# Kernel tuning notes

Hardware: AMD Instinct MI355X
Metric: run time of the kernel (lower is better)

The kernel has to match this reference:

```python
import jax, jax.numpy as jnp
import numpy as np

B, NA, NB = 4, 2048, 2048
IN_A, IN_B, OUT, H = 128, 128, 128, 8
DH = OUT // H  # 16
NEG = jnp.float32(-1e30)
SLOPE = jnp.float32(0.01)


def setup_inputs() -> dict:
    key = jax.random.key(0)
    ks = jax.random.split(key, 13)
    s = 0.05
    return {
        "h_A": jax.random.normal(ks[0], (B, NA, IN_A), jnp.float32),
        "h_B": jax.random.normal(ks[1], (B, NB, IN_B), jnp.float32),
        "mask": jax.random.randint(ks[2], (B, NA, NB), 0, 2) > 0,
        # per-head params stacked on a leading head axis
        "WA_w": jax.random.normal(ks[3], (H, IN_A, DH), jnp.float32) * s,
        "WA_b": jax.random.normal(ks[4], (H, DH), jnp.float32) * s,
        "WB_w": jax.random.normal(ks[5], (H, IN_B, DH), jnp.float32) * s,
        "WB_b": jax.random.normal(ks[6], (H, DH), jnp.float32) * s,
        "aA_w": jax.random.normal(ks[7], (H, DH), jnp.float32) * s,
        "aA_b": jax.random.normal(ks[8], (H,), jnp.float32) * s,
        "aB_w": jax.random.normal(ks[9], (H, DH), jnp.float32) * s,
        "aB_b": jax.random.normal(ks[10], (H,), jnp.float32) * s,
        "W_w": jax.random.normal(ks[11], (OUT, OUT), jnp.float32) * s,
        "W_b": jax.random.normal(ks[12], (OUT,), jnp.float32) * s,
    }


def _leaky(x):
    return jnp.where(x >= 0, x, SLOPE * x)


def reference(h_A, h_B, mask, WA_w, WA_b, WB_w, WB_b, aA_w, aA_b, aB_w, aB_b, W_w, W_b):
    # per-head linear projections: [B, H, N, DH]
    z_A = jnp.einsum('bni,hid->bhnd', h_A, WA_w) + WA_b[None, :, None, :]
    z_B = jnp.einsum('bmi,hid->bhmd', h_B, WB_w) + WB_b[None, :, None, :]
    # additive attention logits: [B, H, NA] + [B, H, NB] -> [B, H, NA, NB]
    eA = jnp.einsum('bhnd,hd->bhn', z_A, aA_w) + aA_b[None, :, None]
    eB = jnp.einsum('bhmd,hd->bhm', z_B, aB_w) + aB_b[None, :, None]
    e = eA[:, :, :, None] + eB[:, :, None, :]
    m = mask[:, None, :, :]  # broadcast over heads
    e = jnp.where(m, e, NEG)
    alpha = jax.nn.softmax(_leaky(e), axis=-1)
    alpha = jnp.where(m, alpha, jnp.zeros((), alpha.dtype))
    # weighted aggregation: [B, H, NA, DH]
    out_h = jnp.einsum('bhnm,bhmd->bhnd', alpha, z_B)
    # concat heads -> [B, NA, OUT], final projection
    cat = out_h.transpose(0, 2, 1, 3).reshape(h_A.shape[0], h_A.shape[1], H * DH)
    return cat @ W_w.T + W_b
```

## Files before the change

### kernel.cpp

```cpp
#include <hip/hip_runtime.h>

typedef unsigned short u16;
typedef unsigned int u32;
typedef unsigned char u8;

typedef _Float16 f16x8 __attribute__((ext_vector_type(8)));
typedef _Float16 f16x2 __attribute__((ext_vector_type(2)));
typedef __attribute__((ext_vector_type(4))) float f32x4;


#if __has_builtin(__builtin_amdgcn_sbfe)
#define SEXTBIT(m, j) ((u32)__builtin_amdgcn_sbfe((int)(m), (u32)(j), 1u))
#else
#define SEXTBIT(m, j) ((u32)(((int)((m) << (31 - (j)))) >> 31))
#endif

__global__ __launch_bounds__(256) void kzero(float* __restrict__ out){
  out[blockIdx.x * 256 + threadIdx.x] = 0.f;
}

__global__ __launch_bounds__(256) void kmask_f32(const u32* __restrict__ mw,
                                                 u32* __restrict__ Mb){
  int t = threadIdx.x;
  int lane = t & 63;
  int wid = blockIdx.x * 4 + (t >> 6);
  size_t base = (size_t)wid * 2048;
  for (int i = 0; i < 32; i += 4){
    u32 v0 = mw[base + (size_t)(i + 0) * 64 + lane];
    u32 v1 = mw[base + (size_t)(i + 1) * 64 + lane];
    u32 v2 = mw[base + (size_t)(i + 2) * 64 + lane];
    u32 v3 = mw[base + (size_t)(i + 3) * 64 + lane];
    unsigned long long b0 = __ballot(v0 != 0u);
    unsigned long long b1 = __ballot(v1 != 0u);
    unsigned long long b2 = __ballot(v2 != 0u);
    unsigned long long b3 = __ballot(v3 != 0u);
    if (lane == 0){
      size_t o = base / 32 + (size_t)i * 2;
      *(unsigned long long*)&Mb[o + 0] = b0;
      *(unsigned long long*)&Mb[o + 2] = b1;
      *(unsigned long long*)&Mb[o + 4] = b2;
      *(unsigned long long*)&Mb[o + 6] = b3;
    }
  }
}

__global__ __launch_bounds__(256) void kmask_b8(const void* __restrict__ maskv,
                                                u32* __restrict__ Mb){
  int oid = blockIdx.x * 256 + threadIdx.x;
  u32 bits = 0;
  const uint4* mp = (const uint4*)maskv + (size_t)oid * 2;
  uint4 va = mp[0], vb = mp[1];
  u32 w[8] = {va.x, va.y, va.z, va.w, vb.x, vb.y, vb.z, vb.w};
  #pragma unroll
  for (int q = 0; q < 8; ++q)
    #pragma unroll
    for (int bb = 0; bb < 4; ++bb)
      bits |= ((w[q] >> (8 * bb)) & 255u ? 1u : 0u) << (q * 4 + bb);
  Mb[oid] = bits;
}

__global__ __launch_bounds__(256) void kmask_b16(const void* __restrict__ maskv,
                                                 u32* __restrict__ Mb){
  int oid = blockIdx.x * 256 + threadIdx.x;
  u32 bits = 0;
  const uint4* mp = (const uint4*)maskv + (size_t)oid * 4;
  #pragma unroll
  for (int k = 0; k < 4; ++k){
    uint4 v = mp[k];
    u32 w[4] = {v.x, v.y, v.z, v.w};
    #pragma unroll
    for (int q = 0; q < 4; ++q){
      bits |= ((w[q] & 0xFFFFu) ? 1u : 0u) << (k * 8 + q * 2);
      bits |= ((w[q] >> 16)     ? 1u : 0u) << (k * 8 + q * 2 + 1);
    }
  }
  Mb[oid] = bits;
}

__global__ __launch_bounds__(256) void kmask_det(const void* __restrict__ maskv,
                                                 u32* __restrict__ Mb){
  __shared__ int s_aw, s_ab, s_ah;
  int t = threadIdx.x;
  if (t == 0){ s_aw = 1; s_ab = 1; s_ah = 1; }
  __syncthreads();
  {
    const u32* mw = (const u32*)maskv;
    int aw = 1, ah = 1, ab = 1;
    #pragma unroll
    for (int j = 0; j < 4; ++j){
      u32 m = mw[t + 256 * j];
      if (!(m == 0u || m == 1u || m == 0x3F800000u)) aw = 0;
      u32 lo = m & 0xFFFFu, hi = m >> 16;
      if (!((lo == 0u || lo == 1u || lo == 0x3F80u) && (hi == 0u || hi == 1u || hi == 0x3F80u))) ah = 0;
      if (m & ~0x01010101u) ab = 0;
    }
    unsigned long long fa = __ballot(!aw);
    unsigned long long fh = __ballot(!ah);
    unsigned long long fb = __ballot(!ab);
    if ((t & 63) == 0){
      if (fa) atomicAnd(&s_aw, 0);
      if (fh) atomicAnd(&s_ah, 0);
      if (fb) atomicAnd(&s_ab, 0);
    }
  }
  __syncthreads();
  int Fm = 0;
  if (s_aw) Fm = 0; else if (s_ab) Fm = 1; else if (s_ah) Fm = 2;

  if (Fm == 0){
    int lane = t & 63;
    int wid = blockIdx.x * 4 + (t >> 6);
    const u32* mw = (const u32*)maskv;
    size_t base = (size_t)wid * 2048;
    for (int i = 0; i < 32; i += 4){
      u32 v0 = mw[base + (size_t)(i + 0) * 64 + lane];
      u32 v1 = mw[base + (size_t)(i + 1) * 64 + lane];
      u32 v2 = mw[base + (size_t)(i + 2) * 64 + lane];
      u32 v3 = mw[base + (size_t)(i + 3) * 64 + lane];
      unsigned long long b0 = __ballot(v0 != 0u);
      unsigned long long b1 = __ballot(v1 != 0u);
      unsigned long long b2 = __ballot(v2 != 0u);
      unsigned long long b3 = __ballot(v3 != 0u);
      if (lane == 0){
        size_t o = base / 32 + (size_t)i * 2;
        *(unsigned long long*)&Mb[o + 0] = b0;
        *(unsigned long long*)&Mb[o + 2] = b1;
        *(unsigned long long*)&Mb[o + 4] = b2;
        *(unsigned long long*)&Mb[o + 6] = b3;
      }
    }
    return;
  }
  int oid = blockIdx.x * 256 + t;
  u32 bits = 0;
  if (Fm == 1){
    const uint4* mp = (const uint4*)maskv + (size_t)oid * 2;
    #pragma unroll
    for (int k = 0; k < 2; ++k){
      uint4 v = mp[k];
      u32 w[4] = {v.x, v.y, v.z, v.w};
      #pragma unroll
      for (int q = 0; q < 4; ++q)
        #pragma unroll
        for (int bb = 0; bb < 4; ++bb)
          bits |= ((w[q] >> (8*bb)) & 255u ? 1u : 0u) << (k*16 + q*4 + bb);
    }
  } else {
    const uint4* mp = (const uint4*)maskv + (size_t)oid * 4;
    #pragma unroll
    for (int k = 0; k < 4; ++k){
      uint4 v = mp[k];
      u32 w[4] = {v.x, v.y, v.z, v.w};
      #pragma unroll
      for (int q = 0; q < 4; ++q){
        bits |= ((w[q] & 0xFFFFu) ? 1u : 0u) << (k*8 + q*2);
        bits |= ((w[q] >> 16)     ? 1u : 0u) << (k*8 + q*2 + 1);
      }
    }
  }
  Mb[oid] = bits;
}

__global__ __launch_bounds__(256) void kprep(
    const float* __restrict__ hA, const float* __restrict__ hB,
    const float* __restrict__ WAw, const float* __restrict__ WAb,
    const float* __restrict__ aAw, const float* __restrict__ aAb,
    const float* __restrict__ WBw, const float* __restrict__ WBb,
    const float* __restrict__ aBw, const float* __restrict__ aBb,
    const float* __restrict__ Ww, float* __restrict__ WtO,
    uint4* __restrict__ zF,
    float* __restrict__ RA,
    u32* __restrict__ EBh, u32* __restrict__ GBh){
  __shared__ float smem[12416];
  int gid = blockIdx.x, t = threadIdx.x;

  if (gid < 256){
    float* h_l = smem;
    float* W_l = smem + 4224;
    float* T   = smem + 4224;
    int R0 = gid * 32;

    for (int j = 0; j < 4; ++j){
      int idx4 = t + 256 * j;
      int r = idx4 >> 5, k0 = (idx4 & 31) * 4;
      *(float4*)&h_l[r * 132 + k0] = *(const float4*)&hB[(size_t)(R0 + r) * 128 + k0];
    }

    int cg = t & 15, rg = t >> 4;
    float acc[2][8];
    for (int i = 0; i < 2; ++i) for (int s = 0; s < 8; ++s) acc[i][s] = 0.f;

    for (int kc = 0; kc < 2; ++kc){
      __syncthreads();
      for (int j = 0; j < 8; ++j){
        int idx4 = t + 256 * j;
        int k = idx4 >> 5, c0 = (idx4 & 31) * 4;
        *(float4*)&W_l[k * 128 + c0] =
          *(const float4*)&WBw[(size_t)(c0 >> 4) * 2048 + (kc * 64 + k) * 16 + (c0 & 15)];
      }
      __syncthreads();
      for (int k = 0; k < 64; ++k){
        int kk = kc * 64 + k;
        float4 w0 = *(const float4*)&W_l[k * 128 + cg * 8];
        float4 w1 = *(const float4*)&W_l[k * 128 + cg * 8 + 4];
        float wv[8] = {w0.x, w0.y, w0.z, w0.w, w1.x, w1.y, w1.z, w1.w};
        #pragma unroll
        for (int i = 0; i < 2; ++i){
          float hv = h_l[(rg * 2 + i) * 132 + kk];
          #pragma unroll
          for (int s = 0; s < 8; ++s) acc[i][s] = fmaf(hv, wv[s], acc[i][s]);
        }
      }
    }
    __syncthreads();
    for (int i = 0; i < 2; ++i)
      #pragma unroll
      for (int s = 0; s < 8; ++s)
        T[(cg * 8 + s) * 33 + rg * 2 + i] = acc[i][s] + WBb[cg * 8 + s];
    __syncthreads();

    int b = R0 >> 11;
    int mblk = (R0 & 2047) >> 5;
    for (int it = t; it < 512; it += 256){
      int h = it >> 6, lane = it & 63;
      int d = lane & 15, mq = (lane >> 4) * 8;
      const float* Tp = &T[(h * 16 + d) * 33 + mq];
      u32 wv2[4];
      #pragma unroll
      for (int p = 0; p < 4; ++p){
        union { f16x2 h2; u32 u; } c;
        c.h2 = (f16x2){(_Float16)Tp[p * 2], (_Float16)Tp[p * 2 + 1]};
        wv2[p] = c.u;
      }
      zF[((size_t)((b * 8 + h) * 64) + mblk) * 64 + lane] = make_uint4(wv2[0], wv2[1], wv2[2], wv2[3]);
    }
  } else if (gid < 768){
    float* h_l = smem;
    float* v_l = smem + 4224;
    float* c_l = smem + 5280;
    float* a_l = smem + 5288;
    int ge = gid - 256;
    int X = ge >> 8;
    int r0 = (ge & 255) * 32;
    const float* hp  = X ? hB  : hA;
    const float* Wp  = X ? WBw : WAw;
    const float* Wbp = X ? WBb : WAb;
    const float* awp = X ? aBw : aAw;
    const float* abp = X ? aBb : aAb;

    for (int j = 0; j < 4; ++j){
      int idx4 = t + 256 * j;
      int r = idx4 >> 5, k0 = (idx4 & 31) * 4;
      *(float4*)&h_l[r * 132 + k0] = *(const float4*)&hp[(size_t)(r0 + r) * 128 + k0];
    }
    if (t < 128) a_l[t] = awp[t];
    __syncthreads();
    #pragma unroll
    for (int p = 0; p < 4; ++p){
      int idx = t + 256 * p;
      int h = idx >> 7, i = idx & 127;
      const float* wrow = Wp + (size_t)h * 2048 + i * 16;
      float s = 0.f;
      #pragma unroll
      for (int d = 0; d < 16; ++d) s = fmaf(wrow[d], a_l[h * 16 + d], s);
      v_l[h * 132 + i] = s;
    }
    if (t < 8){
      float s = abp[t];
      #pragma unroll
      for (int d = 0; d < 16; ++d) s = fmaf(Wbp[t * 16 + d], a_l[t * 16 + d], s);
      c_l[t] = s;
    }
    __syncthreads();

    int r = t >> 3, h = t & 7;
    float acc = c_l[h];
    #pragma unroll
    for (int k0 = 0; k0 < 128; k0 += 4){
      float4 hv = *(const float4*)&h_l[r * 132 + k0];
      float4 vv = *(const float4*)&v_l[h * 132 + k0];
      acc = fmaf(hv.x, vv.x, acc); acc = fmaf(hv.y, vv.y, acc);
      acc = fmaf(hv.z, vv.z, acc); acc = fmaf(hv.w, vv.w, acc);
    }
    int row = r0 + r;
    int b = row >> 11, n = row & 2047;
    if (X){
      float e0 = __expf(acc), e1 = __expf(0.01f * acc);
      float p0 = __shfl_xor(e0, 8, 64);
      float p1 = __shfl_xor(e1, 8, 64);
      if ((((t & 63) >> 3) & 1) == 0){
        union { f16x2 h2; u32 u; } c0, c1;
        c0.h2 = (f16x2){(_Float16)e0, (_Float16)p0};
        c1.h2 = (f16x2){(_Float16)e1, (_Float16)p1};
        u32 di = (u32)((b * 8 + h) * 1024 + (n >> 1));
        EBh[di] = c0.u;
        GBh[di] = c1.u;
      }
    } else {
      RA[(size_t)(b * 8 + h) * 2048 + n] = __expf(-0.99f * acc);
    }
  } else {
    int j = gid - 768;
    int idx = j * 256 + t;
    int c = idx >> 7, o = idx & 127;
    WtO[idx] = Ww[o * 128 + c];
  }
}

__global__ __launch_bounds__(256) void kattn(const uint4* __restrict__ zF,
                                             const float* __restrict__ RA,
                                             const u32* __restrict__ EBh, const u32* __restrict__ GBh,
                                             const u32* __restrict__ Mb,
                                             float* __restrict__ cat){
  __shared__ u32 EB_l[1024];
  __shared__ u32 GB_l[1024];
  __shared__ u32 MR_l[32 * 65];
  u32* Mb_l = MR_l;
  float (*red)[32][17] = (float(*)[32][17])MR_l;
  int t = threadIdx.x;
  int w = t >> 6, lane = t & 63;
  int gid = blockIdx.x;
  int h  = gid & 7;
  int nt = (gid >> 3) & 63;
  int b  = gid >> 9;
  int n0 = nt * 32;
  int nl = lane & 15, q = lane >> 4, qs = q * 8;

  {
    const uint4* src0 = (const uint4*)(EBh + (size_t)(b * 8 + h) * 1024);
    const uint4* src1 = (const uint4*)(GBh + (size_t)(b * 8 + h) * 1024);
    ((uint4*)EB_l)[t] = src0[t];
    ((uint4*)GB_l)[t] = src1[t];
    const uint4* ms = (const uint4*)(Mb + ((size_t)b * 2048 + n0) * 64);
    uint4 m0v = ms[t * 2], m1v = ms[t * 2 + 1];
    int rr = t >> 3, cc = (t & 7) * 8;
    u32* dst = Mb_l + rr * 65 + cc;
    dst[0] = m0v.x; dst[1] = m0v.y; dst[2] = m0v.z; dst[3] = m0v.w;
    dst[4] = m1v.x; dst[5] = m1v.y; dst[6] = m1v.z; dst[7] = m1v.w;
  }

  size_t ebase = (size_t)(b * 8 + h) * 2048;
  float ra0 = RA[ebase + n0 + nl];
  float ra1 = RA[ebase + n0 + 16 + nl];
  f16x2 rho0_2 = (f16x2){(_Float16)ra0, (_Float16)ra0};
  f16x2 rho1_2 = (f16x2){(_Float16)ra1, (_Float16)ra1};

  const u32* EBq = EB_l + w * 256;
  const u32* GBq = GB_l + w * 256;
  const u32* Mrow0 = Mb_l + nl * 65 + w * 16;
  const u32* Mrow1 = Mb_l + (nl + 16) * 65 + w * 16;
  const uint4* zFp = zF + ((size_t)(b * 8 + h) * 64 + w * 16) * 64 + lane;

  f32x4 acc0 = {0.f,0.f,0.f,0.f}, acc1 = {0.f,0.f,0.f,0.f};
  f32x4 lcc0 = {0.f,0.f,0.f,0.f}, lcc1 = {0.f,0.f,0.f,0.f};
  union { u32 u[4]; f16x8 v; } onesu;
  onesu.u[0] = 0x3C003C00u; onesu.u[1] = 0x3C003C00u;
  onesu.u[2] = 0x3C003C00u; onesu.u[3] = 0x3C003C00u;
  const f16x8 ones = onesu.v;

  __syncthreads();

  uint4 Azu, Bzu;
  #define LOADA(sp) do{ Azu = zFp[(size_t)(sp) * 64]; }while(0)
  #define LOADB(sp) do{ Bzu = zFp[(size_t)(sp) * 64]; }while(0)
  #define COMP(sp,ZU_) do{ \
    uint4 EB_ = *(const uint4*)(EBq + (sp) * 16 + q * 4); \
    uint4 GB_ = *(const uint4*)(GBq + (sp) * 16 + q * 4); \
    u32 mb0 = Mrow0[sp] >> qs; \
    u32 mb1 = Mrow1[sp] >> qs; \
    u32 ebu[4] = {EB_.x, EB_.y, EB_.z, EB_.w}; \
    u32 gbu[4] = {GB_.x, GB_.y, GB_.z, GB_.w}; \
    union { u32 u[4]; f16x8 v; } a0, a1; \
    _Pragma("unroll") \
    for (int p = 0; p < 4; ++p){ \
      int j0 = 2*p, j1 = 2*p + 1; \
      u32 k00 = SEXTBIT(mb0, j0); \
      u32 k01 = SEXTBIT(mb0, j1); \
      u32 k10 = SEXTBIT(mb1, j0); \
      u32 k11 = SEXTBIT(mb1, j1); \
      u32 kc0 = __builtin_amdgcn_perm(k01, k00, 0x05040100u); \
      u32 kc1 = __builtin_amdgcn_perm(k11, k10, 0x05040100u); \
      union { u32 u; f16x2 h2; } eb, gb, r0u, r1u; \
      eb.u = ebu[p]; gb.u = gbu[p]; \
      r0u.h2 = __builtin_elementwise_max(eb.h2, rho0_2 * gb.h2); \
      r1u.h2 = __builtin_elementwise_max(eb.h2, rho1_2 * gb.h2); \
      a0.u[p] = r0u.u & kc0; \
      a1.u[p] = r1u.u & kc1; \
    } \
    union { uint4 u; f16x8 v; } zu; zu.u = ZU_; \
    acc0 = __builtin_amdgcn_mfma_f32_16x16x32_f16(a0.v, zu.v, acc0, 0, 0, 0); \
    lcc0 = __builtin_amdgcn_mfma_f32_16x16x32_f16(a0.v, ones, lcc0, 0, 0, 0); \
    acc1 = __builtin_amdgcn_mfma_f32_16x16x32_f16(a1.v, zu.v, acc1, 0, 0, 0); \
    lcc1 = __builtin_amdgcn_mfma_f32_16x16x32_f16(a1.v, ones, lcc1, 0, 0, 0); }while(0)

  LOADA(0);
  LOADB(1);
  #pragma unroll 4
  for (int s = 0; s < 16; s += 2){
    COMP(s, Azu);
    LOADA(s + 2);
    COMP(s + 1, Bzu);
    LOADB(s + 3);
  }
  #undef LOADA
  #undef LOADB
  #undef COMP

  __syncthreads();
  if (w > 0){
    #pragma unroll
    for (int r = 0; r < 4; ++r){
      int row = q * 4 + r;
      red[w - 1][row][nl]      = acc0[r];
      red[w - 1][row + 16][nl] = acc1[r];
    }
    if (nl == 0){
      #pragma unroll
      for (int r = 0; r < 4; ++r){
        red[w - 1][q * 4 + r][16]      = lcc0[r];
        red[w - 1][q * 4 + r + 16][16] = lcc1[r];
      }
    }
  }
  __syncthreads();
  if (w == 0){
    #pragma unroll
    for (int r = 0; r < 4; ++r){
      int row = q * 4 + r;
      float a0 = acc0[r] + red[0][row][nl]      + red[1][row][nl]      + red[2][row][nl];
      float a1 = acc1[r] + red[0][row + 16][nl] + red[1][row + 16][nl] + red[2][row + 16][nl];
      float L0 = lcc0[r] + red[0][row][16]      + red[1][row][16]      + red[2][row][16];
      float L1 = lcc1[r] + red[0][row + 16][16] + red[1][row + 16][16] + red[2][row + 16][16];
      float r0 = (L0 > 0.f) ? 1.f / L0 : 0.f;
      float r1 = (L1 > 0.f) ? 1.f / L1 : 0.f;
      cat[((size_t)(b * 2048) + n0 + row)      * 128 + h * 16 + nl] = a0 * r0;
      cat[((size_t)(b * 2048) + n0 + 16 + row) * 128 + h * 16 + nl] = a1 * r1;
    }
  }
}

__global__ __launch_bounds__(256) void kout(const float* __restrict__ cat,
                                            const float* __restrict__ WtO, const float* __restrict__ Wb,
                                            float* __restrict__ out){
  __shared__ float cat_l[32 * 132];
  __shared__ float Wt_l[64 * 128];
  int R0 = blockIdx.x * 32;
  int t = threadIdx.x;

  for (int jj = 0; jj < 4; ++jj){
    int idx4 = t + 256 * jj;
    int r = idx4 >> 5, c0 = (idx4 & 31) * 4;
    *(float4*)&cat_l[r * 132 + c0] = *(const float4*)&cat[((size_t)R0 + r) * 128 + c0];
  }

  int og = t & 15, rg = t >> 4;
  float acc[2][8];
  for (int i = 0; i < 2; ++i) for (int s = 0; s < 8; ++s) acc[i][s] = 0.f;

  for (int kc = 0; kc < 2; ++kc){
    __syncthreads();
    for (int j = 0; j < 8; ++j){
      int idx4 = t + 256 * j;
      int k = idx4 >> 5, o0 = (idx4 & 31) * 4;
      *(float4*)&Wt_l[k * 128 + o0] = *(const float4*)&WtO[(kc * 64 + k) * 128 + o0];
    }
    __syncthreads();
    for (int k = 0; k < 64; ++k){
      int kk = kc * 64 + k;
      float4 w0 = *(const float4*)&Wt_l[k * 128 + og * 8];
      float4 w1 = *(const float4*)&Wt_l[k * 128 + og * 8 + 4];
      float wv[8] = {w0.x, w0.y, w0.z, w0.w, w1.x, w1.y, w1.z, w1.w};
      #pragma unroll
      for (int i = 0; i < 2; ++i){
        float cv = cat_l[(rg * 2 + i) * 132 + kk];
        #pragma unroll
        for (int s = 0; s < 8; ++s) acc[i][s] = fmaf(cv, wv[s], acc[i][s]);
      }
    }
  }

  for (int i = 0; i < 2; ++i){
    int r = rg * 2 + i;
    float* op = out + (size_t)(R0 + r) * 128 + og * 8;
    *(float4*)(op)     = make_float4(acc[i][0]+Wb[og*8+0], acc[i][1]+Wb[og*8+1], acc[i][2]+Wb[og*8+2], acc[i][3]+Wb[og*8+3]);
    *(float4*)(op + 4) = make_float4(acc[i][4]+Wb[og*8+4], acc[i][5]+Wb[og*8+5], acc[i][6]+Wb[og*8+6], acc[i][7]+Wb[og*8+7]);
  }
}

extern "C" void kernel_launch(void* const* d_in, const int* in_sizes, int n_in,
                              void* d_out, int out_size, void* d_ws, size_t ws_size,
                              hipStream_t stream) {
  const float* hA  = (const float*)d_in[0];
  const float* hB  = (const float*)d_in[1];
  const void* maskv= d_in[2];
  const float* WAw = (const float*)d_in[3];
  const float* WAb = (const float*)d_in[4];
  const float* WBw = (const float*)d_in[5];
  const float* WBb = (const float*)d_in[6];
  const float* aAw = (const float*)d_in[7];
  const float* aAb = (const float*)d_in[8];
  const float* aBw = (const float*)d_in[9];
  const float* aBb = (const float*)d_in[10];
  const float* Ww  = (const float*)d_in[11];
  const float* Wb  = (const float*)d_in[12];

  float* ws   = (float*)d_ws;
  uint4* zF   = (uint4*)ws;
  float* RA   = ws + 524288;
  u32*  EBh   = (u32*)(ws + 655360);
  u32*  GBh   = (u32*)(ws + 720896);
  float* WtO  = ws + 802816;
  u32*  Mb    = (u32*)(ws + 821272);
  float* cat  = ws + 1345560;

  if (ws_size < 2394136ull * 4ull){
    kzero<<<4096, 256, 0, stream>>>((float*)d_out);
    return;
  }

  const long long ME = 4ll * 2048 * 2048;
  long long hsz = in_sizes[0];
  long long msz = in_sizes[2];
  bool bytes_known = (hsz == 4ll * 2048 * 128 * 4);
  if (bytes_known && msz == ME)
    kmask_b8 <<<2048, 256, 0, stream>>>(maskv, Mb);
  else if (bytes_known && msz == 2 * ME)
    kmask_b16<<<2048, 256, 0, stream>>>(maskv, Mb);
  else if (bytes_known && msz == 4 * ME)
    kmask_f32<<<2048, 256, 0, stream>>>((const u32*)maskv, Mb);
  else
    kmask_det<<<2048, 256, 0, stream>>>(maskv, Mb);

  kprep<<< 832, 256, 0, stream>>>(hA, hB,
                                  WAw, WAb, aAw, aAb,
                                  WBw, WBb, aBw, aBb,
                                  Ww, WtO, zF, RA, EBh, GBh);
  kattn<<<2048, 256, 0, stream>>>(zF, RA, EBh, GBh, Mb, cat);
  kout <<< 256, 256, 0, stream>>>(cat, WtO, Wb, (float*)d_out);
}
```

Before: 163.0 us.

## Shrink LDS in prep and output kernels, add MFMA priority hints

The prep kernel's shared buffer is shrunk by staging the weight tile in 32-row chunks over four passes and reusing the input tile region for the transpose buffer, which should allow more blocks per CU. The output projection kernel is rewritten to process 8 rows per block with each thread computing 4 outputs, reading weights directly from global memory over 1024 blocks instead of 256. The attention kernel raises wave priority around its MFMA group, and the mask-format detector now checks one word per thread instead of four. The trade-offs are more synchronisation passes in prep, more global weight traffic in the output kernel, and a smaller sample for mask-format detection.

```diff
diff --git a/kernel.cpp b/kernel.cpp
--- a/kernel.cpp
+++ b/kernel.cpp
@@ -85,15 +85,11 @@
   __syncthreads();
   {
     const u32* mw = (const u32*)maskv;
-    int aw = 1, ah = 1, ab = 1;
-    #pragma unroll
-    for (int j = 0; j < 4; ++j){
-      u32 m = mw[t + 256 * j];
-      if (!(m == 0u || m == 1u || m == 0x3F800000u)) aw = 0;
-      u32 lo = m & 0xFFFFu, hi = m >> 16;
-      if (!((lo == 0u || lo == 1u || lo == 0x3F80u) && (hi == 0u || hi == 1u || hi == 0x3F80u))) ah = 0;
-      if (m & ~0x01010101u) ab = 0;
-    }
+    u32 m = mw[t];
+    int aw = (m == 0u || m == 1u || m == 0x3F800000u);
+    u32 lo = m & 0xFFFFu, hi = m >> 16;
+    int ah = ((lo == 0u || lo == 1u || lo == 0x3F80u) && (hi == 0u || hi == 1u || hi == 0x3F80u));
+    int ab = ((m & ~0x01010101u) == 0u);
     unsigned long long fa = __ballot(!aw);
     unsigned long long fh = __ballot(!ah);
     unsigned long long fb = __ballot(!ab);
@@ -171,13 +167,13 @@
     uint4* __restrict__ zF,
     float* __restrict__ RA,
     u32* __restrict__ EBh, u32* __restrict__ GBh){
-  __shared__ float smem[12416];
+  __shared__ float smem[8320];
   int gid = blockIdx.x, t = threadIdx.x;
 
   if (gid < 256){
     float* h_l = smem;
     float* W_l = smem + 4224;
-    float* T   = smem + 4224;
+    float* T   = smem;
     int R0 = gid * 32;
 
     for (int j = 0; j < 4; ++j){
@@ -190,17 +186,17 @@
     float acc[2][8];
     for (int i = 0; i < 2; ++i) for (int s = 0; s < 8; ++s) acc[i][s] = 0.f;
 
-    for (int kc = 0; kc < 2; ++kc){
+    for (int kc = 0; kc < 4; ++kc){
       __syncthreads();
-      for (int j = 0; j < 8; ++j){
+      for (int j = 0; j < 4; ++j){
         int idx4 = t + 256 * j;
         int k = idx4 >> 5, c0 = (idx4 & 31) * 4;
         *(float4*)&W_l[k * 128 + c0] =
-          *(const float4*)&WBw[(size_t)(c0 >> 4) * 2048 + (kc * 64 + k) * 16 + (c0 & 15)];
+          *(const float4*)&WBw[(size_t)(c0 >> 4) * 2048 + (kc * 32 + k) * 16 + (c0 & 15)];
       }
       __syncthreads();
-      for (int k = 0; k < 64; ++k){
-        int kk = kc * 64 + k;
+      for (int k = 0; k < 32; ++k){
+        int kk = kc * 32 + k;
         float4 w0 = *(const float4*)&W_l[k * 128 + cg * 8];
         float4 w1 = *(const float4*)&W_l[k * 128 + cg * 8 + 4];
         float wv[8] = {w0.x, w0.y, w0.z, w0.w, w1.x, w1.y, w1.z, w1.w};
@@ -388,10 +384,12 @@
       a1.u[p] = r1u.u & kc1; \
     } \
     union { uint4 u; f16x8 v; } zu; zu.u = ZU_; \
+    __builtin_amdgcn_s_setprio(1); \
     acc0 = __builtin_amdgcn_mfma_f32_16x16x32_f16(a0.v, zu.v, acc0, 0, 0, 0); \
     lcc0 = __builtin_amdgcn_mfma_f32_16x16x32_f16(a0.v, ones, lcc0, 0, 0, 0); \
     acc1 = __builtin_amdgcn_mfma_f32_16x16x32_f16(a1.v, zu.v, acc1, 0, 0, 0); \
-    lcc1 = __builtin_amdgcn_mfma_f32_16x16x32_f16(a1.v, ones, lcc1, 0, 0, 0); }while(0)
+    lcc1 = __builtin_amdgcn_mfma_f32_16x16x32_f16(a1.v, ones, lcc1, 0, 0, 0); \
+    __builtin_amdgcn_s_setprio(0); }while(0)
 
   LOADA(0);
   LOADB(1);
@@ -442,49 +440,31 @@
 __global__ __launch_bounds__(256) void kout(const float* __restrict__ cat,
                                             const float* __restrict__ WtO, const float* __restrict__ Wb,
                                             float* __restrict__ out){
-  __shared__ float cat_l[32 * 132];
-  __shared__ float Wt_l[64 * 128];
-  int R0 = blockIdx.x * 32;
+  __shared__ float cat_l[8 * 132];
+  int R0 = blockIdx.x * 8;
   int t = threadIdx.x;
 
-  for (int jj = 0; jj < 4; ++jj){
-    int idx4 = t + 256 * jj;
-    int r = idx4 >> 5, c0 = (idx4 & 31) * 4;
-    *(float4*)&cat_l[r * 132 + c0] = *(const float4*)&cat[((size_t)R0 + r) * 128 + c0];
-  }
-
-  int og = t & 15, rg = t >> 4;
-  float acc[2][8];
-  for (int i = 0; i < 2; ++i) for (int s = 0; s < 8; ++s) acc[i][s] = 0.f;
-
-  for (int kc = 0; kc < 2; ++kc){
-    __syncthreads();
-    for (int j = 0; j < 8; ++j){
-      int idx4 = t + 256 * j;
-      int k = idx4 >> 5, o0 = (idx4 & 31) * 4;
-      *(float4*)&Wt_l[k * 128 + o0] = *(const float4*)&WtO[(kc * 64 + k) * 128 + o0];
-    }
-    __syncthreads();
-    for (int k = 0; k < 64; ++k){
-      int kk = kc * 64 + k;
-      float4 w0 = *(const float4*)&Wt_l[k * 128 + og * 8];
-      float4 w1 = *(const float4*)&Wt_l[k * 128 + og * 8 + 4];
-      float wv[8] = {w0.x, w0.y, w0.z, w0.w, w1.x, w1.y, w1.z, w1.w};
-      #pragma unroll
-      for (int i = 0; i < 2; ++i){
-        float cv = cat_l[(rg * 2 + i) * 132 + kk];
-        #pragma unroll
-        for (int s = 0; s < 8; ++s) acc[i][s] = fmaf(cv, wv[s], acc[i][s]);
-      }
-    }
-  }
-
-  for (int i = 0; i < 2; ++i){
-    int r = rg * 2 + i;
-    float* op = out + (size_t)(R0 + r) * 128 + og * 8;
-    *(float4*)(op)     = make_float4(acc[i][0]+Wb[og*8+0], acc[i][1]+Wb[og*8+1], acc[i][2]+Wb[og*8+2], acc[i][3]+Wb[og*8+3]);
-    *(float4*)(op + 4) = make_float4(acc[i][4]+Wb[og*8+4], acc[i][5]+Wb[og*8+5], acc[i][6]+Wb[og*8+6], acc[i][7]+Wb[og*8+7]);
-  }
+  {
+    int r = t >> 5, k0 = (t & 31) * 4;
+    *(float4*)&cat_l[r * 132 + k0] = *(const float4*)&cat[((size_t)R0 + r) * 128 + k0];
+  }
+  __syncthreads();
+
+  int r  = t >> 5;
+  int c0 = (t & 31) * 4;
+  float4 bv = *(const float4*)&Wb[c0];
+  float a0 = bv.x, a1 = bv.y, a2 = bv.z, a3 = bv.w;
+  const float* cr = &cat_l[r * 132];
+  #pragma unroll 8
+  for (int k = 0; k < 128; ++k){
+    float cv = cr[k];
+    float4 wv = *(const float4*)&WtO[k * 128 + c0];
+    a0 = fmaf(cv, wv.x, a0);
+    a1 = fmaf(cv, wv.y, a1);
+    a2 = fmaf(cv, wv.z, a2);
+    a3 = fmaf(cv, wv.w, a3);
+  }
+  *(float4*)&out[((size_t)R0 + r) * 128 + c0] = make_float4(a0, a1, a2, a3);
 }
 
 extern "C" void kernel_launch(void* const* d_in, const int* in_sizes, int n_in,
@@ -536,5 +516,5 @@
                                   WBw, WBb, aBw, aBb,
                                   Ww, WtO, zF, RA, EBh, GBh);
   kattn<<<2048, 256, 0, stream>>>(zF, RA, EBh, GBh, Mb, cat);
-  kout <<< 256, 256, 0, stream>>>(cat, WtO, Wb, (float*)d_out);
-}
+  kout <<<1024, 256, 0, stream>>>(cat, WtO, Wb, (float*)d_out);
+}
```

Result: slower. 170.4 us (+4.6%).
